# Kernel optimization log

Measured on AMD Instinct MI355X. Metric: run time of the kernel, lower is better.

Reference implementation:

```python
import jax, jax.numpy as jnp
import numpy as np


def setup_inputs() -> dict:
    key = jax.random.key(0)
    k1, k2, k3 = jax.random.split(key, 3)
    B, S, F, K = 4096, 256, 64, 16  # batch, seq_len, n_features, n_snippets
    L = S  # snippet length == size_seq
    x = jax.random.normal(k1, (B, S, F), dtype=jnp.float32)
    W_cls = jax.random.normal(k2, (F, S, K), dtype=jnp.float32) / np.sqrt(S)
    snippet_list = jax.random.normal(k3, (F, K, L), dtype=jnp.float32)
    return {"x": x, "W_cls": W_cls, "snippet_list": snippet_list}


def reference(x, W_cls, snippet_list):
    # Replace NaNs with 0 (x[x != x] = 0 in torch)
    x = jnp.where(jnp.isnan(x), jnp.zeros_like(x), x)
    # classifier on x.transpose(2,1): [B,S,F] -> [B,F,S] -> logits [B,K,F]
    logits = jnp.einsum('bsf,fsk->bkf', x, W_cls)
    # argmax over snippet axis -> idx [B, F]
    idx = jnp.argmax(logits, axis=1)
    F = snippet_list.shape[0]
    # fused batched gather: result[b, f, :] = snippet_list[f, idx[b, f]]
    snip = snippet_list[jnp.arange(F)[None, :], idx]  # [B, F, L]
    return snip
```

## Files before the change

kernel.cpp:

```cpp
#include <hip/hip_runtime.h>
#include <stdint.h>

constexpr int Bn = 4096, Sn = 256, Fn = 64, Kn = 16;

__global__ void transpose_w_kernel(const float* __restrict__ W, float* __restrict__ Wl) {
  int t = blockIdx.x * 256 + threadIdx.x;
  int r = t & 3, f = (t >> 2) & 63, kq = (t >> 8) & 3, s = t >> 10;
  Wl[t] = W[(f * Sn + s) * Kn + kq * 4 + r];
}

__device__ __forceinline__ void gld_lds16(const float4* g, float4* l) {
  __builtin_amdgcn_global_load_lds(
      (const __attribute__((address_space(1))) uint32_t*)g,
      (__attribute__((address_space(3))) uint32_t*)l, 16, 0, 0);
}

__global__ __launch_bounds__(256, 2) void gemm_argmax_kernel(
    const float* __restrict__ x, const float4* __restrict__ Wl4,
    int* __restrict__ idxg) {
  __shared__ float4 Wbuf[2][2048];

  const int tid = threadIdx.x;
  const int lane = tid & 63;
  const int w = tid >> 6;
  const int b0 = blockIdx.x * 8 + w * 2;
  const size_t xrow = (size_t)Sn * Fn;
  const float* xb0 = x + (size_t)b0 * xrow + lane;

  float acc[2][16];
#pragma unroll
  for (int j = 0; j < 2; ++j)
#pragma unroll
    for (int k = 0; k < 16; ++k) acc[j][k] = 0.f;

  float xA[8][2], xB[8][2];

#define STAGEW(c, p)                                                         \
  {                                                                          \
    const float4* _src = Wl4 + (size_t)(c) * 2048 + (w * 8) * 64 + lane;     \
    float4* _dst = &Wbuf[p][(w * 8) * 64];                                   \
    _Pragma("unroll") for (int ii = 0; ii < 8; ++ii)                         \
        gld_lds16(_src + ii * 64, _dst + ii * 64);                           \
  }

#define LOADX(c, xn)                                                         \
  {                                                                          \
    _Pragma("unroll") for (int s8 = 0; s8 < 8; ++s8)                         \
        _Pragma("unroll") for (int j = 0; j < 2; ++j)                        \
            xn[s8][j] = xb0[(size_t)j * xrow + (size_t)((c) * 8 + s8) * Fn]; \
  }

#define COMPUTE(p, xn)                                                       \
  {                                                                          \
    _Pragma("unroll") for (int s8 = 0; s8 < 8; ++s8) {                       \
      float4 wq[4];                                                          \
      _Pragma("unroll") for (int kq = 0; kq < 4; ++kq)                       \
          wq[kq] = Wbuf[p][(s8 * 4 + kq) * 64 + lane];                       \
      float xv[2];                                                           \
      _Pragma("unroll") for (int j = 0; j < 2; ++j) {                        \
        float v = xn[s8][j];                                                 \
        xv[j] = (v == v) ? v : 0.f;                                          \
      }                                                                      \
      float wv[16];                                                          \
      _Pragma("unroll") for (int kq = 0; kq < 4; ++kq) {                     \
        wv[4 * kq + 0] = wq[kq].x; wv[4 * kq + 1] = wq[kq].y;                \
        wv[4 * kq + 2] = wq[kq].z; wv[4 * kq + 3] = wq[kq].w;                \
      }                                                                      \
      _Pragma("unroll") for (int j = 0; j < 2; ++j)                          \
          _Pragma("unroll") for (int k = 0; k < 16; ++k)                     \
              acc[j][k] = fmaf(xv[j], wv[k], acc[j][k]);                     \
    }                                                                        \
  }

  STAGEW(0, 0);
  LOADX(0, xA);
  __syncthreads();

  for (int cc = 0; cc < 32; cc += 2) {
    STAGEW(cc + 1, 1);
    LOADX(cc + 1, xB);
    COMPUTE(0, xA);
    __syncthreads();
    if (cc + 2 < 32) {
      STAGEW(cc + 2, 0);
      LOADX(cc + 2, xA);
    }
    COMPUTE(1, xB);
    __syncthreads();
  }

#pragma unroll
  for (int j = 0; j < 2; ++j) {
    float bv = acc[j][0];
    int bk = 0;
#pragma unroll
    for (int k = 1; k < 16; ++k)
      if (acc[j][k] > bv) { bv = acc[j][k]; bk = k; }
    idxg[(b0 + j) * 64 + lane] = bk;
  }
#undef STAGEW
#undef LOADX
#undef COMPUTE
}

__global__ __launch_bounds__(256) void gather_kernel(
    const int* __restrict__ idxg, const float4* __restrict__ snip4,
    float4* __restrict__ out4) {
  const int lane = threadIdx.x & 63;
  const int gw = (blockIdx.x * 256 + threadIdx.x) >> 6;
  const int r0 = gw * 16;
  int kk[16];
#pragma unroll
  for (int i = 0; i < 16; ++i) kk[i] = idxg[r0 + i];
#pragma unroll
  for (int i = 0; i < 16; ++i) {
    const int r = r0 + i;
    const int f = r & 63;
    out4[(size_t)r * 64 + lane] = snip4[(size_t)((f * Kn + kk[i]) * 64) + lane];
  }
}

__global__ __launch_bounds__(256, 2) void fused_fallback(
    const float* __restrict__ x, const float* __restrict__ Wsrc,
    const float4* __restrict__ snip4, float4* __restrict__ out4) {
  __shared__ int idxs[8][64];
  const int tid = threadIdx.x;
  const int lane = tid & 63;
  const int w = tid >> 6;
  const int bbase = blockIdx.x * 8;
  const int b0 = bbase + w * 2;
  const size_t xrow = (size_t)Sn * Fn;

  float acc0[16], acc1[16];
#pragma unroll
  for (int k = 0; k < 16; ++k) { acc0[k] = 0.f; acc1[k] = 0.f; }
  const float* pc0 = x + (size_t)b0 * xrow + lane;
  const float* pc1 = pc0 + xrow;
  float xc0[8], xc1[8], xn0[8], xn1[8];
#pragma unroll
  for (int j = 0; j < 8; ++j) { xn0[j] = pc0[j * 64]; xn1[j] = pc1[j * 64]; }
  for (int c = 0; c < 32; ++c) {
#pragma unroll
    for (int j = 0; j < 8; ++j) {
      float v0 = xn0[j], v1 = xn1[j];
      xc0[j] = (v0 == v0) ? v0 : 0.f;
      xc1[j] = (v1 == v1) ? v1 : 0.f;
    }
    if (c < 31) {
      pc0 += 512; pc1 += 512;
#pragma unroll
      for (int j = 0; j < 8; ++j) { xn0[j] = pc0[j * 64]; xn1[j] = pc1[j * 64]; }
    }
#pragma unroll
    for (int s8 = 0; s8 < 8; ++s8) {
      const int s = c * 8 + s8;
      float wv[16];
      const float4* wq = reinterpret_cast<const float4*>(Wsrc) + ((size_t)(lane * Sn + s) << 2);
#pragma unroll
      for (int jj = 0; jj < 4; ++jj) {
        float4 q = wq[jj];
        wv[4 * jj + 0] = q.x; wv[4 * jj + 1] = q.y; wv[4 * jj + 2] = q.z; wv[4 * jj + 3] = q.w;
      }
#pragma unroll
      for (int k = 0; k < 16; ++k) {
        acc0[k] = fmaf(xc0[s8], wv[k], acc0[k]);
        acc1[k] = fmaf(xc1[s8], wv[k], acc1[k]);
      }
    }
  }
  {
    float bv0 = acc0[0], bv1 = acc1[0];
    int bk0 = 0, bk1 = 0;
#pragma unroll
    for (int k = 1; k < 16; ++k) {
      if (acc0[k] > bv0) { bv0 = acc0[k]; bk0 = k; }
      if (acc1[k] > bv1) { bv1 = acc1[k]; bk1 = k; }
    }
    idxs[w * 2 + 0][lane] = bk0;
    idxs[w * 2 + 1][lane] = bk1;
  }
  __syncthreads();
#pragma unroll 4
  for (int it = 0; it < 128; ++it) {
    int r = (it << 2) | w;
    int bi = r >> 6, f = r & 63;
    int kk = idxs[bi][f];
    float4 v = snip4[(size_t)((f * Kn + kk) << 6) + lane];
    out4[((size_t)(bbase + bi) * Fn + f) * 64 + lane] = v;
  }
}

extern "C" void kernel_launch(void* const* d_in, const int* in_sizes, int n_in,
                              void* d_out, int out_size, void* d_ws, size_t ws_size,
                              hipStream_t stream) {
  const float* x = (const float*)d_in[0];
  const float* W = (const float*)d_in[1];
  const float* snip = (const float*)d_in[2];
  float4* out4 = (float4*)d_out;
  const float4* snip4 = (const float4*)snip;

  const size_t wl_bytes = (size_t)Sn * Fn * Kn * sizeof(float);
  const size_t idx_bytes = (size_t)Bn * Fn * sizeof(int);
  if (ws_size >= wl_bytes + idx_bytes) {
    float* Wl = (float*)d_ws;
    int* idxg = (int*)((char*)d_ws + wl_bytes);
    transpose_w_kernel<<<(Sn * Fn * Kn) / 256, 256, 0, stream>>>(W, Wl);
    gemm_argmax_kernel<<<Bn / 8, 256, 0, stream>>>(x, (const float4*)Wl, idxg);
    gather_kernel<<<(Bn * Fn) / (4 * 16), 256, 0, stream>>>(idxg, snip4, out4);
  } else {
    fused_fallback<<<Bn / 8, 256, 0, stream>>>(x, W, snip4, out4);
  }
}
```

Before: 141.6 us.

## Split snippet-logit axis across two wave groups with LDS argmax merge

Doubles the GEMM-argmax block to 512 threads. Each pair of waves now handles the same batch rows but a different half of the 16 snippet logits, so each thread keeps 16 accumulators instead of 32. The partial argmaxes are combined through shared memory after an extra barrier. The aim is more resident waves and better latency hiding on the memory-bound x stream. The cost is that each x element is loaded twice, once per half, and there is an added sync plus a small amount of extra LDS.

```diff
diff --git a/kernel.cpp b/kernel.cpp
--- a/kernel.cpp
+++ b/kernel.cpp
@@ -15,31 +15,35 @@
       (__attribute__((address_space(3))) uint32_t*)l, 16, 0, 0);
 }
 
-__global__ __launch_bounds__(256, 2) void gemm_argmax_kernel(
+__global__ __launch_bounds__(512, 4) void gemm_argmax_kernel(
     const float* __restrict__ x, const float4* __restrict__ Wl4,
     int* __restrict__ idxg) {
   __shared__ float4 Wbuf[2][2048];
+  __shared__ float bval[8][64];
+  __shared__ int bidx[8][64];
 
   const int tid = threadIdx.x;
   const int lane = tid & 63;
   const int w = tid >> 6;
-  const int b0 = blockIdx.x * 8 + w * 2;
+  const int wb = w & 3;
+  const int wk = w >> 2;
+  const int b0 = blockIdx.x * 8 + wb * 2;
   const size_t xrow = (size_t)Sn * Fn;
   const float* xb0 = x + (size_t)b0 * xrow + lane;
 
-  float acc[2][16];
+  float acc[2][8];
 #pragma unroll
   for (int j = 0; j < 2; ++j)
 #pragma unroll
-    for (int k = 0; k < 16; ++k) acc[j][k] = 0.f;
+    for (int k = 0; k < 8; ++k) acc[j][k] = 0.f;
 
   float xA[8][2], xB[8][2];
 
 #define STAGEW(c, p)                                                         \
   {                                                                          \
-    const float4* _src = Wl4 + (size_t)(c) * 2048 + (w * 8) * 64 + lane;     \
-    float4* _dst = &Wbuf[p][(w * 8) * 64];                                   \
-    _Pragma("unroll") for (int ii = 0; ii < 8; ++ii)                         \
+    const float4* _src = Wl4 + (size_t)(c) * 2048 + w * 256 + lane;          \
+    float4* _dst = &Wbuf[p][w * 256];                                        \
+    _Pragma("unroll") for (int ii = 0; ii < 4; ++ii)                         \
         gld_lds16(_src + ii * 64, _dst + ii * 64);                           \
   }
 
@@ -53,21 +57,18 @@
 #define COMPUTE(p, xn)                                                       \
   {                                                                          \
     _Pragma("unroll") for (int s8 = 0; s8 < 8; ++s8) {                       \
-      float4 wq[4];                                                          \
-      _Pragma("unroll") for (int kq = 0; kq < 4; ++kq)                       \
-          wq[kq] = Wbuf[p][(s8 * 4 + kq) * 64 + lane];                       \
+      float4 wq0 = Wbuf[p][(s8 * 4 + wk * 2 + 0) * 64 + lane];               \
+      float4 wq1 = Wbuf[p][(s8 * 4 + wk * 2 + 1) * 64 + lane];               \
       float xv[2];                                                           \
       _Pragma("unroll") for (int j = 0; j < 2; ++j) {                        \
         float v = xn[s8][j];                                                 \
         xv[j] = (v == v) ? v : 0.f;                                          \
       }                                                                      \
-      float wv[16];                                                          \
-      _Pragma("unroll") for (int kq = 0; kq < 4; ++kq) {                     \
-        wv[4 * kq + 0] = wq[kq].x; wv[4 * kq + 1] = wq[kq].y;                \
-        wv[4 * kq + 2] = wq[kq].z; wv[4 * kq + 3] = wq[kq].w;                \
-      }                                                                      \
+      float wv[8];                                                           \
+      wv[0] = wq0.x; wv[1] = wq0.y; wv[2] = wq0.z; wv[3] = wq0.w;            \
+      wv[4] = wq1.x; wv[5] = wq1.y; wv[6] = wq1.z; wv[7] = wq1.w;            \
       _Pragma("unroll") for (int j = 0; j < 2; ++j)                          \
-          _Pragma("unroll") for (int k = 0; k < 16; ++k)                     \
+          _Pragma("unroll") for (int k = 0; k < 8; ++k)                      \
               acc[j][k] = fmaf(xv[j], wv[k], acc[j][k]);                     \
     }                                                                        \
   }
@@ -89,14 +90,34 @@
     __syncthreads();
   }
 
+  float bv[2];
+  int bk[2];
 #pragma unroll
   for (int j = 0; j < 2; ++j) {
-    float bv = acc[j][0];
-    int bk = 0;
-#pragma unroll
-    for (int k = 1; k < 16; ++k)
-      if (acc[j][k] > bv) { bv = acc[j][k]; bk = k; }
-    idxg[(b0 + j) * 64 + lane] = bk;
+    bv[j] = acc[j][0];
+    int lk = 0;
+#pragma unroll
+    for (int k = 1; k < 8; ++k)
+      if (acc[j][k] > bv[j]) { bv[j] = acc[j][k]; lk = k; }
+    bk[j] = wk * 8 + lk;
+  }
+
+  if (wk == 1) {
+#pragma unroll
+    for (int j = 0; j < 2; ++j) {
+      bval[wb * 2 + j][lane] = bv[j];
+      bidx[wb * 2 + j][lane] = bk[j];
+    }
+  }
+  __syncthreads();
+  if (wk == 0) {
+#pragma unroll
+    for (int j = 0; j < 2; ++j) {
+      float v1 = bval[wb * 2 + j][lane];
+      int k1 = bidx[wb * 2 + j][lane];
+      int fin = (v1 > bv[j]) ? k1 : bk[j];
+      idxg[(b0 + j) * 64 + lane] = fin;
+    }
   }
 #undef STAGEW
 #undef LOADX
@@ -205,7 +226,7 @@
     float* Wl = (float*)d_ws;
     int* idxg = (int*)((char*)d_ws + wl_bytes);
     transpose_w_kernel<<<(Sn * Fn * Kn) / 256, 256, 0, stream>>>(W, Wl);
-    gemm_argmax_kernel<<<Bn / 8, 256, 0, stream>>>(x, (const float4*)Wl, idxg);
+    gemm_argmax_kernel<<<Bn / 8, 512, 0, stream>>>(x, (const float4*)Wl, idxg);
     gather_kernel<<<(Bn * Fn) / (4 * 16), 256, 0, stream>>>(idxg, snip4, out4);
   } else {
     fused_fallback<<<Bn / 8, 256, 0, stream>>>(x, W, snip4, out4);
```

New measurement: 235.9 us. 66.5% more time.
